# Optimization experiments

Hardware: AMD Instinct MI355X
Metric: run time of the kernel (lower is better)

Reference implementation:

```python
import jax, jax.numpy as jnp
import numpy as np

HAND_PARAM_DIM = 32
MASK_THRESHOLD = 0.5
MAX_SAMPLES = 1024
INF_DIST = 1.0e6
EPS = 1e-8

B, S, HW, V = 4, 16, 65536, 778


def setup_inputs() -> dict:
    key = jax.random.key(0)
    ks = jax.random.split(key, 10)
    return {
        "hand_params": jax.random.normal(ks[0], (B, S, 2 * HAND_PARAM_DIM), jnp.float32),
        "gs_means": jax.random.normal(ks[1], (B, S, HW, 3), jnp.float32),
        "hand_gs_mask": jax.random.uniform(ks[2], (B, S, HW), jnp.float32),
        "hand_valid": jax.random.randint(ks[3], (B, S, 2), 0, 2).astype(jnp.int32),
        "v_template_l": jax.random.normal(ks[4], (V, 3), jnp.float32),
        "v_template_r": jax.random.normal(ks[5], (V, 3), jnp.float32),
        "shapedirs_l": jax.random.normal(ks[6], (V, 3, 10), jnp.float32) * 0.1,
        "shapedirs_r": jax.random.normal(ks[7], (V, 3, 10), jnp.float32) * 0.1,
        "posedirs_l": jax.random.normal(ks[8], (V, 3, 15), jnp.float32) * 0.1,
        "posedirs_r": jax.random.normal(ks[9], (V, 3, 15), jnp.float32) * 0.1,
    }


def quat_wxyz_to_rotvec(q):
    # q: [..., 4] (w, x, y, z) -> rotvec [..., 3]; faithful to the torch impl.
    q_norm = jnp.sqrt(jnp.sum(q * q, axis=-1, keepdims=True) + EPS)
    q = q / jnp.maximum(q_norm, EPS)
    w = q[..., 0:1]
    xyz = q[..., 1:4]
    sign = jnp.where(w < 0, -1.0, 1.0)
    w = w * sign
    xyz = xyz * sign
    sin_half = jnp.sqrt(jnp.sum(xyz * xyz, axis=-1, keepdims=True) + EPS)
    w_safe = jnp.clip(w, -1.0 + EPS, 1.0 - EPS)
    angle = 2.0 * jnp.arctan2(sin_half, w_safe)
    factor = jnp.where(sin_half < 1e-6, 2.0, angle / jnp.maximum(sin_half, EPS))
    return xyz * factor


def _rodrigues(pts, rotvec):
    # pts: [N, V, 3], rotvec: [N, 3]
    angle = jnp.sqrt(jnp.sum(rotvec * rotvec, axis=-1, keepdims=True) + EPS)  # [N,1]
    axis = rotvec / angle                                                      # [N,3]
    c = jnp.cos(angle)[:, None, :]   # [N,1,1]
    s = jnp.sin(angle)[:, None, :]
    k = axis[:, None, :]             # [N,1,3]
    kxv = jnp.cross(jnp.broadcast_to(k, pts.shape), pts)
    kdv = jnp.sum(k * pts, axis=-1, keepdims=True)
    return pts * c + kxv * s + k * kdv * (1.0 - c)


def _mano_points(p, v_template, shapedirs, posedirs):
    # p: [N, 32] -> points [N, V, 3] (linear MANO surrogate: template + blend dirs,
    # globally rotated by quaternion->rotvec and translated).
    transl = p[:, :3]
    q = p[:, 3:7]
    hand_pose = p[:, 7:22]
    betas = p[:, 22:32]
    rotvec = quat_wxyz_to_rotvec(q)
    pts = (v_template[None]
           + jnp.einsum('vck,nk->nvc', shapedirs, betas)
           + jnp.einsum('vck,nk->nvc', posedirs, hand_pose))
    return _rodrigues(pts, rotvec) + transl[:, None, :]


def reference(hand_params, gs_means, hand_gs_mask, hand_valid,
              v_template_l, v_template_r, shapedirs_l, shapedirs_r,
              posedirs_l, posedirs_r):
    b, s = hand_params.shape[:2]
    hw = gs_means.shape[2]
    bs = b * s
    params_flat = hand_params.reshape(bs, 2, HAND_PARAM_DIM)
    hv = hand_valid.reshape(bs, 2).astype(bool)

    left_pts = _mano_points(params_flat[:, 0], v_template_l, shapedirs_l, posedirs_l)
    right_pts = _mano_points(params_flat[:, 1], v_template_r, shapedirs_r, posedirs_r)
    left_pts = jnp.where(hv[:, 0:1, None], left_pts, INF_DIST)
    right_pts = jnp.where(hv[:, 1:2, None], right_pts, INF_DIST)
    mesh_pts = jnp.concatenate([left_pts, right_pts], axis=1)   # [BS, 2V, 3]

    k = min(MAX_SAMPLES, hw)
    mask_flat = hand_gs_mask.reshape(bs, hw)
    means_flat = gs_means.reshape(bs, hw, 3)
    top_vals, top_idx = jax.lax.top_k(mask_flat, k)             # [BS, K]
    sel_valid = (top_vals > MASK_THRESHOLD) & jnp.any(hv, axis=-1, keepdims=True)
    sampled = jnp.take_along_axis(means_flat, top_idx[..., None], axis=1)  # [BS, K, 3]

    # squared euclidean distances via gram trick: [BS, K, 2V]
    sa = jnp.sum(sampled * sampled, axis=-1)
    sb = jnp.sum(mesh_pts * mesh_pts, axis=-1)
    d2 = jnp.maximum(sa[:, :, None] + sb[:, None, :]
                     - 2.0 * jnp.einsum('nkc,npc->nkp', sampled, mesh_pts), 0.0)
    nn_d2 = jnp.min(d2, axis=-1)                                 # [BS, K]

    w = sel_valid.astype(nn_d2.dtype)
    num_samples = jnp.maximum(jnp.sum(w), 1.0)
    return jnp.sum(nn_d2 * w) / num_samples
```

## Files before the change

kernel.cpp:

```cpp
#include <hip/hip_runtime.h>
#include <math.h>

#define HAND_PARAM_DIM 32
#define INF_DIST 1000000.0f
#define EPS 1e-8f
#define NROW 64
#define HW_N 65536
#define NV 778
#define NMESH 1556
#define NMESH_PAD 1568
#define SLICE 98
#define NSLICE 16
#define K_SEL 1024u
#define HALF_BITS  0x3F000000u
#define GUESS_BITS 0x3F733333u
#define TOP_BITS   0x3F800000u
#define CHUNK_SLOT 512
#define CAND_MAX   8192
#define FIX_SCALE 4294967296.0

#define OFF_CAND 0u
#define OFF_CCNT 4194304u
#define OFF_CTR  4198400u
#define OFF_MESH 4198416u
#define OFF_SAMP 5804048u
#define OFF_MINP 6852624u

typedef unsigned long long u64;

__global__ void __launch_bounds__(256) combo_kernel(
    const float* __restrict__ mask, const int* __restrict__ hv,
    u64* __restrict__ cand, unsigned* __restrict__ ccnt,
    const float* __restrict__ hp,
    const float* __restrict__ vtl, const float* __restrict__ vtr,
    const float* __restrict__ sdl, const float* __restrict__ sdr,
    const float* __restrict__ pdl, const float* __restrict__ pdr,
    float4* __restrict__ meshP)
{
    int blk = blockIdx.x;
    int t = threadIdx.x;

    if (blk < 1024) {
        __shared__ u64 loc[CHUNK_SLOT];
        __shared__ unsigned nc, nbad;
        int row = blk >> 4, chunk = blk & 15;
        if (!(hv[row*2] | hv[row*2+1])) return;
        if (t == 0) { nc = 0u; nbad = 0u; }
        __syncthreads();
        const float4* m4 = (const float4*)(mask + (size_t)row * HW_N + chunk * 4096);
#pragma unroll
        for (int k = 0; k < 4; k++) {
            float4 v = m4[k*256 + t];
            unsigned e0 = (unsigned)(chunk*4096 + (k*256 + t)*4);
            unsigned u;
#define PROC(comp, off_) { u = __float_as_uint(comp); \
            if (u >= GUESS_BITS) { \
                unsigned p_ = atomicAdd(&nc, 1u); \
                if (p_ < CHUNK_SLOT) loc[p_] = ((u64)u << 32) | (e0 + off_); \
                if (u >= TOP_BITS) nbad = 1u; } }
            PROC(v.x, 0u) PROC(v.y, 1u) PROC(v.z, 2u) PROC(v.w, 3u)
#undef PROC
        }
        __syncthreads();
        unsigned n = (nc < CHUNK_SLOT) ? nc : CHUNK_SLOT;
        if (t == 0) ccnt[row*16 + chunk] = nc | (nbad << 31);
        u64* dst = cand + ((size_t)(row*16 + chunk)) * CHUNK_SLOT;
        for (unsigned i = t; i < n; i += 256) dst[i] = loc[i];
        return;
    }

    int mb   = blk - 1024;
    int row  = mb >> 1;
    int hand = mb & 1;
    const float* p = hp + row * (2 * HAND_PARAM_DIM) + hand * HAND_PARAM_DIM;
    int valid = hv[row * 2 + hand];

    const float* vt = hand ? vtr : vtl;
    const float* sd = hand ? sdr : sdl;
    const float* pd = hand ? pdr : pdl;

    if (hand == 1 && t < (NMESH_PAD - NMESH))
        meshP[row * NMESH_PAD + NMESH + t] = make_float4(0.f, 0.f, 0.f, 3.4e38f);

    float tx = p[0], ty = p[1], tz = p[2];
    float q0 = p[3], q1 = p[4], q2 = p[5], q3 = p[6];
    float qn = sqrtf(q0*q0 + q1*q1 + q2*q2 + q3*q3 + EPS);
    float inv = 1.0f / fmaxf(qn, EPS);
    q0 *= inv; q1 *= inv; q2 *= inv; q3 *= inv;
    float sgn = (q0 < 0.0f) ? -1.0f : 1.0f;
    q0 *= sgn; q1 *= sgn; q2 *= sgn; q3 *= sgn;
    float sin_half = sqrtf(q1*q1 + q2*q2 + q3*q3 + EPS);
    float w_safe = fminf(fmaxf(q0, -1.0f + EPS), 1.0f - EPS);
    float ang2 = 2.0f * atan2f(sin_half, w_safe);
    float factor = (sin_half < 1e-6f) ? 2.0f : ang2 / fmaxf(sin_half, EPS);
    float rx = q1 * factor, ry = q2 * factor, rz = q3 * factor;
    float ang = sqrtf(rx*rx + ry*ry + rz*rz + EPS);
    float iang = 1.0f / ang;
    float ax = rx * iang, ay = ry * iang, az = rz * iang;
    float c = cosf(ang), s = sinf(ang), omc = 1.0f - c;

    float pose[15], betas[10];
#pragma unroll
    for (int k = 0; k < 15; k++) pose[k] = p[7 + k];
#pragma unroll
    for (int k = 0; k < 10; k++) betas[k] = p[22 + k];

    for (int v = t; v < NV; v += 256) {
        float px = vt[v*3+0], py = vt[v*3+1], pz = vt[v*3+2];
        const float* sdv = sd + v * 30;
#pragma unroll
        for (int k = 0; k < 10; k++) {
            px = fmaf(sdv[k],      betas[k], px);
            py = fmaf(sdv[10 + k], betas[k], py);
            pz = fmaf(sdv[20 + k], betas[k], pz);
        }
        const float* pdv = pd + v * 45;
#pragma unroll
        for (int k = 0; k < 15; k++) {
            px = fmaf(pdv[k],      pose[k], px);
            py = fmaf(pdv[15 + k], pose[k], py);
            pz = fmaf(pdv[30 + k], pose[k], pz);
        }
        float cx = ay * pz - az * py;
        float cy = az * px - ax * pz;
        float cz = ax * py - ay * px;
        float kdv = ax * px + ay * py + az * pz;
        float ox = px * c + cx * s + ax * kdv * omc + tx;
        float oy = py * c + cy * s + ay * kdv * omc + ty;
        float oz = pz * c + cz * s + az * kdv * omc + tz;
        if (!valid) { ox = INF_DIST; oy = INF_DIST; oz = INF_DIST; }
        float sb = fmaf(ox, ox, fmaf(oy, oy, oz * oz));
        meshP[row * NMESH_PAD + hand * NV + v] = make_float4(-2.0f*ox, -2.0f*oy, -2.0f*oz, sb);
    }
}

__global__ void __launch_bounds__(256) sel_fin_kernel(
    const float* __restrict__ mask, const float* __restrict__ means,
    const int* __restrict__ hv,
    const u64* __restrict__ cand, const unsigned* __restrict__ ccnt,
    float4* __restrict__ sampbuf, unsigned* __restrict__ ctr)
{
    __shared__ unsigned cval[CAND_MAX], cidx[CAND_MAX];
    __shared__ unsigned h[256], seg[256];
    __shared__ unsigned csub[16], cbase[16];
    __shared__ unsigned sbin, sRn, sbad, stot;
    __shared__ unsigned tlist[256];
    __shared__ unsigned tn, ns, scut;
    int row = blockIdx.x, t = threadIdx.x;

    if (row == 0 && t < 4) ctr[t] = 0u;
    for (unsigned i = t; i < K_SEL; i += 256)
        sampbuf[(size_t)row * K_SEL + i] = make_float4(0.f, 0.f, 0.f, -1.0f);
    if (!(hv[row*2] | hv[row*2+1])) return;

    if (t == 0) { sbad = 0u; tn = 0u; ns = 0u; }
    __syncthreads();
    if (t < 16) {
        unsigned w = ccnt[row*16 + t];
        unsigned n = w & 0x7FFFFFFFu;
        csub[t] = (n < CHUNK_SLOT) ? n : CHUNK_SLOT;
        if ((w >> 31) || n > CHUNK_SLOT) atomicOr(&sbad, 1u);
    }
    __syncthreads();
    if (t == 0) {
        unsigned run = 0;
#pragma unroll
        for (int c = 0; c < 16; c++) { cbase[c] = run; run += csub[c]; }
        stot = run;
    }
    __syncthreads();
    unsigned cnt = stot;
    bool ok = (sbad == 0u) && (cnt >= K_SEL) && (cnt <= CAND_MAX);
    const float* mrow = mask + (size_t)row * HW_N;
    unsigned M = ok ? cnt : (unsigned)HW_N;

    if (ok) {
#pragma unroll
        for (int c = 0; c < 16; c++) {
            unsigned n = csub[c], b = cbase[c];
            const u64* src = cand + ((size_t)(row*16 + c)) * CHUNK_SLOT;
            for (unsigned i = t; i < n; i += 256) {
                u64 e = src[i];
                cval[b + i] = (unsigned)(e >> 32); cidx[b + i] = (unsigned)e;
            }
        }
    }
    __syncthreads();

    unsigned T, R;
    if (ok) {
        unsigned pfx = 0u; R = K_SEL;
        for (int ph = 0; ph < 2; ph++) {
            int sh = 8 * (1 - ph);
            h[t] = 0u;
            __syncthreads();
            for (unsigned i = t; i < cnt; i += 256) {
                unsigned off = cval[i] - GUESS_BITS;
                if (ph == 0 || (off >> 8) == pfx) atomicAdd(&h[(off >> sh) & 0xFFu], 1u);
            }
            __syncthreads();
            seg[t] = h[t];
            __syncthreads();
            for (int off2 = 1; off2 < 256; off2 <<= 1) {
                unsigned v = (t + off2 < 256) ? seg[t + off2] : 0u;
                __syncthreads(); seg[t] += v; __syncthreads();
            }
            unsigned excl = (t < 255) ? seg[t + 1] : 0u;
            if (excl < R && R <= seg[t]) { sbin = (unsigned)t; sRn = R - excl; }
            __syncthreads();
            pfx = (ph == 0) ? sbin : ((pfx << 8) | sbin);
            R = sRn;
            __syncthreads();
        }
        T = GUESS_BITS + pfx;
    } else {
        unsigned pfx = 0u; R = K_SEL;
        for (int ph = 0; ph < 4; ph++) {
            int sh = 24 - 8 * ph;
            unsigned pm = (ph == 0) ? 0u : (0xFFFFFFFFu << (sh + 8));
            h[t] = 0u;
            __syncthreads();
            for (unsigned i = t; i < M; i += 256) {
                unsigned u = __float_as_uint(mrow[i]);
                if ((u & pm) == pfx) atomicAdd(&h[(u >> sh) & 0xFFu], 1u);
            }
            __syncthreads();
            seg[t] = h[t];
            __syncthreads();
            for (int off2 = 1; off2 < 256; off2 <<= 1) {
                unsigned v = (t + off2 < 256) ? seg[t + off2] : 0u;
                __syncthreads(); seg[t] += v; __syncthreads();
            }
            unsigned excl = (t < 255) ? seg[t + 1] : 0u;
            if (excl < R && R <= seg[t]) { sbin = (unsigned)t; sRn = R - excl; }
            __syncthreads();
            pfx |= sbin << sh;
            R = sRn;
            __syncthreads();
        }
        T = pfx;
    }

    for (unsigned i = t; i < M; i += 256) {
        unsigned u = ok ? cval[i] : __float_as_uint(mrow[i]);
        if (u == T) {
            unsigned p = atomicAdd(&tn, 1u);
            if (p < 256u) tlist[p] = ok ? cidx[i] : i;
        }
    }
    __syncthreads();
    if (t == 0) {
        unsigned n2 = (tn < 256u) ? tn : 256u;
        for (unsigned a = 1; a < n2; a++) {
            unsigned key = tlist[a]; int b = (int)a - 1;
            while (b >= 0 && tlist[b] > key) { tlist[b+1] = tlist[b]; b--; }
            tlist[b+1] = key;
        }
        unsigned r = R;
        if (r > n2) r = n2;
        if (r < 1u) r = 1u;
        scut = (n2 > 0u) ? tlist[r - 1] : 0u;
    }
    __syncthreads();
    unsigned cut = scut;
    for (unsigned i = t; i < M; i += 256) {
        unsigned u  = ok ? cval[i] : __float_as_uint(mrow[i]);
        unsigned id = ok ? cidx[i] : i;
        if (u > T || (u == T && id <= cut)) {
            unsigned p = atomicAdd(&ns, 1u);
            if (p < K_SEL) {
                const float* gm = means + ((size_t)row * HW_N + id) * 3;
                float sx = gm[0], sy = gm[1], sz = gm[2];
                float sa = fmaf(sx, sx, fmaf(sy, sy, sz * sz));
                float w  = (u > HALF_BITS) ? sa : -1.0f;
                sampbuf[(size_t)row * K_SEL + p] = make_float4(sx, sy, sz, w);
            }
        }
    }
}

__global__ void __launch_bounds__(256) dist_kernel(
    const float4* __restrict__ meshP, const float4* __restrict__ sampbuf,
    float* __restrict__ minpart)
{
    __shared__ float4 mq[SLICE];
    int blk = blockIdx.x;
    int r = blk & 63, sl = blk >> 6;
    int t = threadIdx.x;

    if (t < SLICE) mq[t] = meshP[r * NMESH_PAD + sl * SLICE + t];

    const float4* sb = sampbuf + (size_t)r * K_SEL;
    float sx[4], sy[4], sz[4], mn[4];
#pragma unroll
    for (int k = 0; k < 4; k++) {
        float4 s = sb[t + 256*k];
        sx[k] = s.x; sy[k] = s.y; sz[k] = s.z;
        mn[k] = 3.4e38f;
    }
    __syncthreads();

#pragma unroll 2
    for (int i = 0; i < SLICE; i++) {
        float4 a = mq[i];
#pragma unroll
        for (int k = 0; k < 4; k++)
            mn[k] = fminf(mn[k], fmaf(sx[k], a.x, fmaf(sy[k], a.y, fmaf(sz[k], a.z, a.w))));
    }

    float* mp = minpart + ((size_t)r * NSLICE + sl) * K_SEL;
#pragma unroll
    for (int k = 0; k < 4; k++) mp[t + 256*k] = mn[k];
}

__global__ void __launch_bounds__(256) reduce_kernel(
    const float* __restrict__ minpart, const float4* __restrict__ sampbuf,
    unsigned* __restrict__ ctr, float* __restrict__ out)
{
    __shared__ long long rs[256];
    __shared__ unsigned rc[256];
    int row = blockIdx.x;
    int t = threadIdx.x;

    long long acc = 0; unsigned c = 0;
#pragma unroll
    for (int k = 0; k < 4; k++) {
        int j = k * 256 + t;
        const float* mp = minpart + (size_t)row * NSLICE * K_SEL + j;
        float m = mp[0];
#pragma unroll
        for (int s = 1; s < NSLICE; s++) m = fminf(m, mp[s * (int)K_SEL]);
        float4 sp = sampbuf[(size_t)row * K_SEL + j];
        if (sp.w >= 0.0f) {
            float d2 = fmaxf(m + sp.w, 0.0f);
            acc += (long long)((double)d2 * FIX_SCALE);
            c += 1u;
        }
    }
    rs[t] = acc; rc[t] = c;
    __syncthreads();
    for (int off = 128; off > 0; off >>= 1) {
        if (t < off) { rs[t] += rs[t+off]; rc[t] += rc[t+off]; }
        __syncthreads();
    }
    if (t == 0) {
        atomicAdd((u64*)ctr, (u64)rs[0]);
        atomicAdd(&ctr[2], rc[0]);
        __threadfence();
        unsigned tk = atomicAdd(&ctr[3], 1u);
        if (tk == (unsigned)(NROW - 1)) {
            u64 sbits = atomicAdd((u64*)ctr, 0ull);
            unsigned cc = atomicAdd(&ctr[2], 0u);
            double sum = (double)(long long)sbits / FIX_SCALE;
            out[0] = (float)(sum / (double)(cc ? cc : 1u));
        }
    }
}

extern "C" void kernel_launch(void* const* d_in, const int* in_sizes, int n_in,
                              void* d_out, int out_size, void* d_ws, size_t ws_size,
                              hipStream_t stream) {
    const float* hp    = (const float*)d_in[0];
    const float* means = (const float*)d_in[1];
    const float* mask  = (const float*)d_in[2];
    const int*   hv    = (const int*)  d_in[3];
    const float* vtl   = (const float*)d_in[4];
    const float* vtr   = (const float*)d_in[5];
    const float* sdl   = (const float*)d_in[6];
    const float* sdr   = (const float*)d_in[7];
    const float* pdl   = (const float*)d_in[8];
    const float* pdr   = (const float*)d_in[9];
    float* out = (float*)d_out;

    char* ws = (char*)d_ws;
    u64*      cand    = (u64*)(ws + OFF_CAND);
    unsigned* ccnt    = (unsigned*)(ws + OFF_CCNT);
    unsigned* ctr     = (unsigned*)(ws + OFF_CTR);
    float4*   meshP   = (float4*)(ws + OFF_MESH);
    float4*   sampbuf = (float4*)(ws + OFF_SAMP);
    float*    minpart = (float*)(ws + OFF_MINP);

    combo_kernel<<<1024 + 128, 256, 0, stream>>>(mask, hv, cand, ccnt,
                                                 hp, vtl, vtr, sdl, sdr, pdl, pdr, meshP);
    sel_fin_kernel<<<NROW, 256, 0, stream>>>(mask, means, hv, cand, ccnt, sampbuf, ctr);
    dist_kernel<<<NROW * NSLICE, 256, 0, stream>>>(meshP, sampbuf, minpart);
    reduce_kernel<<<NROW, 256, 0, stream>>>(minpart, sampbuf, ctr, out);
}
```

Baseline: 49.79 us.

## Fuse distance min and final reduction into one kernel with packed atomic accumulator

The distance kernel now gives each block 64 samples against the full mesh, which is held in shared memory and split across four thread groups. Partial minima are combined in shared memory, and the per-sample result goes straight into a packed 64-bit atomic holding a fixed-point sum and a count, so the separate reduce kernel and the minpart buffer are no longer needed. This saves one launch and a global round trip. In exchange it clamps d2 at 2000, uses coarser fixed-point precision and relies on a last-block completion counter, which could alter numerics.

```diff
diff --git a/kernel.cpp b/kernel.cpp
--- a/kernel.cpp
+++ b/kernel.cpp
@@ -9,22 +9,20 @@
 #define NV 778
 #define NMESH 1556
 #define NMESH_PAD 1568
-#define SLICE 98
-#define NSLICE 16
+#define QPTS 392
 #define K_SEL 1024u
 #define HALF_BITS  0x3F000000u
 #define GUESS_BITS 0x3F733333u
 #define TOP_BITS   0x3F800000u
 #define CHUNK_SLOT 512
 #define CAND_MAX   8192
-#define FIX_SCALE 4294967296.0
+#define FIX2 65536.0f
 
 #define OFF_CAND 0u
 #define OFF_CCNT 4194304u
 #define OFF_CTR  4198400u
 #define OFF_MESH 4198416u
 #define OFF_SAMP 5804048u
-#define OFF_MINP 6852624u
 
 typedef unsigned long long u64;
 
@@ -281,78 +279,53 @@
 
 __global__ void __launch_bounds__(256) dist_kernel(
     const float4* __restrict__ meshP, const float4* __restrict__ sampbuf,
-    float* __restrict__ minpart)
+    u64* __restrict__ gpack, unsigned* __restrict__ done,
+    float* __restrict__ out)
 {
-    __shared__ float4 mq[SLICE];
+    __shared__ float4 mq[NMESH_PAD];
+    __shared__ float redm[256];
     int blk = blockIdx.x;
-    int r = blk & 63, sl = blk >> 6;
+    int r = blk & 63, chunk = blk >> 6;
     int t = threadIdx.x;
-
-    if (t < SLICE) mq[t] = meshP[r * NMESH_PAD + sl * SLICE + t];
-
-    const float4* sb = sampbuf + (size_t)r * K_SEL;
-    float sx[4], sy[4], sz[4], mn[4];
-#pragma unroll
-    for (int k = 0; k < 4; k++) {
-        float4 s = sb[t + 256*k];
-        sx[k] = s.x; sy[k] = s.y; sz[k] = s.z;
-        mn[k] = 3.4e38f;
-    }
-    __syncthreads();
-
-#pragma unroll 2
-    for (int i = 0; i < SLICE; i++) {
+    int s = t & 63, q = t >> 6;
+
+    for (int i = t; i < NMESH_PAD; i += 256) mq[i] = meshP[r * NMESH_PAD + i];
+
+    float4 sp = sampbuf[(size_t)r * K_SEL + chunk * 64 + s];
+    float mn = 3.4e38f;
+    __syncthreads();
+
+    const int p0 = q * QPTS;
+#pragma unroll 4
+    for (int i = p0; i < p0 + QPTS; i++) {
         float4 a = mq[i];
-#pragma unroll
-        for (int k = 0; k < 4; k++)
-            mn[k] = fminf(mn[k], fmaf(sx[k], a.x, fmaf(sy[k], a.y, fmaf(sz[k], a.z, a.w))));
-    }
-
-    float* mp = minpart + ((size_t)r * NSLICE + sl) * K_SEL;
-#pragma unroll
-    for (int k = 0; k < 4; k++) mp[t + 256*k] = mn[k];
-}
-
-__global__ void __launch_bounds__(256) reduce_kernel(
-    const float* __restrict__ minpart, const float4* __restrict__ sampbuf,
-    unsigned* __restrict__ ctr, float* __restrict__ out)
-{
-    __shared__ long long rs[256];
-    __shared__ unsigned rc[256];
-    int row = blockIdx.x;
-    int t = threadIdx.x;
-
-    long long acc = 0; unsigned c = 0;
-#pragma unroll
-    for (int k = 0; k < 4; k++) {
-        int j = k * 256 + t;
-        const float* mp = minpart + (size_t)row * NSLICE * K_SEL + j;
-        float m = mp[0];
-#pragma unroll
-        for (int s = 1; s < NSLICE; s++) m = fminf(m, mp[s * (int)K_SEL]);
-        float4 sp = sampbuf[(size_t)row * K_SEL + j];
+        mn = fminf(mn, fmaf(sp.x, a.x, fmaf(sp.y, a.y, fmaf(sp.z, a.z, a.w))));
+    }
+    redm[t] = mn;
+    __syncthreads();
+
+    if (t < 64) {
+        float m = fminf(fminf(redm[s], redm[s + 64]),
+                        fminf(redm[s + 128], redm[s + 192]));
+        u64 pk = 0ull;
         if (sp.w >= 0.0f) {
             float d2 = fmaxf(m + sp.w, 0.0f);
-            acc += (long long)((double)d2 * FIX_SCALE);
-            c += 1u;
-        }
-    }
-    rs[t] = acc; rc[t] = c;
-    __syncthreads();
-    for (int off = 128; off > 0; off >>= 1) {
-        if (t < off) { rs[t] += rs[t+off]; rc[t] += rc[t+off]; }
-        __syncthreads();
-    }
-    if (t == 0) {
-        atomicAdd((u64*)ctr, (u64)rs[0]);
-        atomicAdd(&ctr[2], rc[0]);
-        __threadfence();
-        unsigned tk = atomicAdd(&ctr[3], 1u);
-        if (tk == (unsigned)(NROW - 1)) {
-            u64 sbits = atomicAdd((u64*)ctr, 0ull);
-            unsigned cc = atomicAdd(&ctr[2], 0u);
-            double sum = (double)(long long)sbits / FIX_SCALE;
-            out[0] = (float)(sum / (double)(cc ? cc : 1u));
+            d2 = fminf(d2, 2000.0f);
+            pk = ((u64)(d2 * FIX2) << 20) | 1ull;
+        }
+#pragma unroll
+        for (int off = 32; off > 0; off >>= 1)
+            pk += __shfl_down(pk, off, 64);
+        if (t == 0) {
+            u64 oldv = atomicAdd(gpack, pk);
+            asm volatile("" :: "v"((unsigned)oldv), "v"((unsigned)(oldv >> 32)) : "memory");
+            unsigned tk = atomicAdd(done, 1u);
+            if (tk == 1023u) {
+                u64 tot = atomicAdd(gpack, 0ull);
+                unsigned cc = (unsigned)(tot & 0xFFFFFull);
+                double sum = (double)(tot >> 20) / (double)FIX2;
+                out[0] = (float)(sum / (double)(cc ? cc : 1u));
+            }
         }
     }
 }
@@ -378,11 +351,10 @@
     unsigned* ctr     = (unsigned*)(ws + OFF_CTR);
     float4*   meshP   = (float4*)(ws + OFF_MESH);
     float4*   sampbuf = (float4*)(ws + OFF_SAMP);
-    float*    minpart = (float*)(ws + OFF_MINP);
 
     combo_kernel<<<1024 + 128, 256, 0, stream>>>(mask, hv, cand, ccnt,
                                                  hp, vtl, vtr, sdl, sdr, pdl, pdr, meshP);
     sel_fin_kernel<<<NROW, 256, 0, stream>>>(mask, means, hv, cand, ccnt, sampbuf, ctr);
-    dist_kernel<<<NROW * NSLICE, 256, 0, stream>>>(meshP, sampbuf, minpart);
-    reduce_kernel<<<NROW, 256, 0, stream>>>(minpart, sampbuf, ctr, out);
+    dist_kernel<<<NROW * 16, 256, 0, stream>>>(meshP, sampbuf,
+                                               (u64*)ctr, ctr + 2, out);
 }
```

Result: slower. 79.61 us (+59.9%).
